# Performance work log

Measured on AMD Instinct MI355X. Metric: run time of the kernel, lower is better.

The kernel has to match this reference:

```python
import jax, jax.numpy as jnp
import numpy as np
from jax import lax

V, H, B, S, NSLOT, T, G, NSW = 20000, 400, 16, 256, 30, 10, 3, 40


def setup_inputs() -> dict:
    key = jax.random.key(0)
    ks = jax.random.split(key, 24)
    p = lambda k, shape: jax.random.normal(k, shape, dtype=jnp.float32) * 0.1
    return {
        'story': jax.random.randint(ks[0], (B, S), 0, V),
        'enc_lens': jax.random.randint(ks[1], (B,), S // 2, S + 1),
        'target_batches': jax.random.randint(ks[2], (B, NSLOT, T), 0, V),
        'domain_idx': jax.random.randint(ks[3], (NSLOT,), 0, NSW),
        'slot_idx': jax.random.randint(ks[4], (NSLOT,), 0, NSW),
        'emb': p(ks[5], (V, H)),
        'enc_Wih_f': p(ks[6], (3 * H, H)), 'enc_Whh_f': p(ks[7], (3 * H, H)),
        'enc_bih_f': p(ks[8], (3 * H,)), 'enc_bhh_f': p(ks[9], (3 * H,)),
        'enc_Wih_b': p(ks[10], (3 * H, H)), 'enc_Whh_b': p(ks[11], (3 * H, H)),
        'enc_bih_b': p(ks[12], (3 * H,)), 'enc_bhh_b': p(ks[13], (3 * H,)),
        'dec_Wih': p(ks[14], (3 * H, H)), 'dec_Whh': p(ks[15], (3 * H, H)),
        'dec_bih': p(ks[16], (3 * H,)), 'dec_bhh': p(ks[17], (3 * H,)),
        'Wr': p(ks[18], (1, 3 * H)), 'br': p(ks[19], (1,)),
        'Wg': p(ks[20], (G, H)), 'bg': p(ks[21], (G,)),
        'slot_table': p(ks[22], (NSW, H)),
    }


def _gru_scan(x, m, h0, Wih, Whh, bih, bhh):
    # x: [S,B,H], m: [S,B] validity mask (packed-sequence semantics)
    def step(h, xm):
        xt, mt = xm
        gi = xt @ Wih.T + bih
        gh = h @ Whh.T + bhh
        ir, iz, inn = jnp.split(gi, 3, -1)
        hr, hz, hn = jnp.split(gh, 3, -1)
        r = jax.nn.sigmoid(ir + hr)
        z = jax.nn.sigmoid(iz + hz)
        n = jnp.tanh(inn + r * hn)
        hnew = (1.0 - z) * n + z * h
        h = jnp.where(mt[:, None], hnew, h)
        y = jnp.where(mt[:, None], hnew, 0.0)
        return h, y
    hT, ys = lax.scan(step, h0, (x, m))
    return ys, hT


def reference(story, enc_lens, target_batches, domain_idx, slot_idx, emb,
              enc_Wih_f, enc_Whh_f, enc_bih_f, enc_bhh_f,
              enc_Wih_b, enc_Whh_b, enc_bih_b, enc_bhh_b,
              dec_Wih, dec_Whh, dec_bih, dec_bhh,
              Wr, br, Wg, bg, slot_table):
    Bc, Sc = story.shape
    nslot = domain_idx.shape[0]
    Tc = target_batches.shape[2]
    NB = nslot * Bc

    # ----- EncoderRNN: bidirectional GRU over story (seq-major) -----
    x = emb[story.T]                                   # [S,B,H]
    mask = jnp.arange(Sc)[:, None] < enc_lens[None, :]  # [S,B]
    h0 = jnp.zeros((Bc, H), jnp.float32)
    ys_f, h_f = _gru_scan(x, mask, h0, enc_Wih_f, enc_Whh_f, enc_bih_f, enc_bhh_f)
    ys_b, h_b = _gru_scan(x[::-1], mask[::-1], h0, enc_Wih_b, enc_Whh_b, enc_bih_b, enc_bhh_b)
    ys_b = ys_b[::-1]
    encoded_outputs = (ys_f + ys_b).transpose(1, 0, 2)  # [B,S,H]
    enc_hidden = h_f + h_b                              # [B,H]

    # ----- Generator (parallel decode, teacher forcing) -----
    combined = slot_table[domain_idx] + slot_table[slot_idx]           # [nslot,H]
    slot_emb_arr = jnp.repeat(combined[:, None, :], Bc, axis=1).reshape(NB, H)
    hidden0 = jnp.tile(enc_hidden, (nslot, 1))                         # [NB,H]
    enc_out = jnp.tile(encoded_outputs, (nslot, 1, 1))                 # [NB,S,H]
    lens_rep = jnp.tile(enc_lens, nslot)
    story_rep = jnp.tile(story, (nslot, 1))                            # [NB,S]
    attn_mask = jnp.arange(Sc)[None, :] < lens_rep[:, None]            # [NB,S]
    rows = jnp.arange(NB)[:, None]

    # teacher-forced decoder inputs: step0 = slot emb, then gold tokens
    tgt_flat = target_batches.transpose(1, 0, 2).reshape(NB, Tc)       # [NB,T]
    dec_in = jnp.concatenate([slot_emb_arr[None], emb[tgt_flat[:, :Tc - 1].T]], axis=0)  # [T,NB,H]

    def dec_step(h, x_in):
        gi = x_in @ dec_Wih.T + dec_bih
        gh = h @ dec_Whh.T + dec_bhh
        ir, iz, inn = jnp.split(gi, 3, -1)
        hr, hz, hn = jnp.split(gh, 3, -1)
        r = jax.nn.sigmoid(ir + hr)
        z = jax.nn.sigmoid(iz + hz)
        n = jnp.tanh(inn + r * hn)
        h = (1.0 - z) * n + z * h                      # dec_state == new hidden
        scores = jnp.einsum('nh,nsh->ns', h, enc_out)
        scores = jnp.where(attn_mask, scores, -jnp.inf)
        prob = jax.nn.softmax(scores, axis=1)          # [NB,S]
        context = jnp.einsum('ns,nsh->nh', prob, enc_out)
        p_vocab = jax.nn.softmax(h @ emb.T, axis=1)    # [NB,V]
        p_gen_vec = jnp.concatenate([h, context, x_in], axis=-1)
        sw = jax.nn.sigmoid(p_gen_vec @ Wr.T + br)     # [NB,1]
        p_ctx = jnp.zeros_like(p_vocab).at[rows, story_rep].add(prob)
        final_p = (1.0 - sw) * p_ctx + sw * p_vocab
        return h, (final_p, context)

    _, (finals, contexts) = lax.scan(dec_step, hidden0, dec_in)
    all_point_outputs = finals.reshape(Tc, nslot, Bc, V).transpose(1, 2, 0, 3)  # [nslot,B,T,V]
    all_gate_outputs = (contexts[0] @ Wg.T + bg).reshape(nslot, Bc, G)
    return all_point_outputs, all_gate_outputs
```

## Files before the change

### kernel.cpp

```cpp
#include <hip/hip_runtime.h>
#include <hip/hip_bf16.h>

typedef unsigned short u16;
typedef __attribute__((ext_vector_type(8))) short bf16x8;
typedef __attribute__((ext_vector_type(4))) float f32x4;
typedef __attribute__((ext_vector_type(4))) unsigned u32x4;

static constexpr int V = 20000, H = 400, B = 16, S = 256, NSLOT = 30, T = 10, G = 3;
static constexpr int H3 = 3 * H;
static constexpr int NB = NSLOT * B;
static constexpr int MM = T * NB;
static constexpr int ENBLK = 20;
static constexpr int ESL   = 20;
static constexpr int EROWS = 64;
static constexpr int EKP   = 416;
static constexpr int ENC_BLOCKS = 2 * ENBLK;
static constexpr int DGI_TM = (MM + 63) / 64;
static constexpr int DGI_TN = (H3 + 63) / 64;
static constexpr int DGI_TILES = DGI_TM * DGI_TN;
static constexpr int DGH_TM = (NB + 63) / 64;
static constexpr int DGH_TN = (H3 + 63) / 64;
static constexpr int DGH_TILES = DGH_TM * DGH_TN;
static constexpr int HP2 = 424;
static constexpr int SCP = 260;
static constexpr int PP  = 264;
static constexpr int CXP = 404;
static constexpr int FUSED_LDS = 32*HP2*2 + 32*SCP*4 + 32*PP*2 + 32*CXP*4;
static constexpr int NE = V * H;
static constexpr int NW = H3 * H;
static constexpr int NP = 2 * ENBLK * EROWS * EKP;

__device__ __forceinline__ float bf2f(u16 v) {
    union { unsigned u; float f; } x; x.u = ((unsigned)v) << 16; return x.f;
}
__device__ __forceinline__ u16 f2bf(float f) {
    union { float f; unsigned u; } x; x.f = f;
    unsigned r = x.u + 0x7fffu + ((x.u >> 16) & 1u);
    return (u16)(r >> 16);
}
__device__ __forceinline__ float sigm(float v) { return 1.f / (1.f + __expf(-v)); }

__global__ __launch_bounds__(256) void gemm_bt(
    const u16* __restrict__ A, const u16* __restrict__ Bt,
    const float* __restrict__ bias, float* __restrict__ C,
    int M, int N, int K, int lda, int ldb, long long ldc)
{
    __shared__ u16 As[64][40];
    __shared__ u16 Bs[64][40];
    const int m0 = blockIdx.x * 64, n0 = blockIdx.y * 64;
    const int tid = threadIdx.x, wave = tid >> 6, lane = tid & 63;
    const int wm = (wave >> 1) * 32, wn = (wave & 1) * 32;
    const int srow = tid >> 2, scol = (tid & 3) * 8;
    const int fr = lane & 15, kq = lane >> 4;
    f32x4 acc[2][2];
#pragma unroll
    for (int i = 0; i < 2; ++i)
#pragma unroll
        for (int j = 0; j < 2; ++j) acc[i][j] = (f32x4){0.f, 0.f, 0.f, 0.f};

    for (int k0 = 0; k0 < K; k0 += 32) {
        {
            int gr = m0 + srow, gc = k0 + scol;
            bf16x8 v = (bf16x8){0,0,0,0,0,0,0,0};
            if (gr < M && gc + 8 <= K) v = *(const bf16x8*)(A + (long long)gr * lda + gc);
            *(bf16x8*)&As[srow][scol] = v;
        }
        {
            int gr = n0 + srow, gc = k0 + scol;
            bf16x8 v = (bf16x8){0,0,0,0,0,0,0,0};
            if (gr < N && gc + 8 <= K) v = *(const bf16x8*)(Bt + (long long)gr * ldb + gc);
            *(bf16x8*)&Bs[srow][scol] = v;
        }
        __syncthreads();
        bf16x8 af[2], bfr[2];
#pragma unroll
// ... 35 lines not shown
    const int M = S * B, N = H3, K = H;

    __shared__ u16 As[64][40];
    __shared__ u16 Bs[64][40];
    const int m0 = blockIdx.x * 64, n0 = blockIdx.y * 64;
    const int tid = threadIdx.x, wave = tid >> 6, lane = tid & 63;
    const int wm = (wave >> 1) * 32, wn = (wave & 1) * 32;
    const int srow = tid >> 2, scol = (tid & 3) * 8;
    const int fr = lane & 15, kq = lane >> 4;
    f32x4 acc[2][2];
#pragma unroll
    for (int i = 0; i < 2; ++i)
#pragma unroll
        for (int j = 0; j < 2; ++j) acc[i][j] = (f32x4){0.f, 0.f, 0.f, 0.f};

    for (int k0 = 0; k0 < K; k0 += 32) {
        {
            int gr = m0 + srow, gc = k0 + scol;
            bf16x8 v = (bf16x8){0,0,0,0,0,0,0,0};
            if (gr < M && gc + 8 <= K) v = *(const bf16x8*)(A + (long long)gr * K + gc);
            *(bf16x8*)&As[srow][scol] = v;
        }
        {
            int gr = n0 + srow, gc = k0 + scol;
            bf16x8 v = (bf16x8){0,0,0,0,0,0,0,0};
            if (gr < N && gc + 8 <= K) v = *(const bf16x8*)(Bt + (long long)gr * K + gc);
            *(bf16x8*)&Bs[srow][scol] = v;
        }
        __syncthreads();
        bf16x8 af[2], bfr[2];
#pragma unroll
        for (int i = 0; i < 2; ++i) af[i]  = *(const bf16x8*)&As[wm + i * 16 + fr][kq * 8];
#pragma unroll
        for (int j = 0; j < 2; ++j) bfr[j] = *(const bf16x8*)&Bs[wn + j * 16 + fr][kq * 8];
#pragma unroll
        for (int i = 0; i < 2; ++i)
#pragma unroll
            for (int j = 0; j < 2; ++j)
                acc[i][j] = __builtin_amdgcn_mfma_f32_16x16x32_bf16(af[i], bfr[j], acc[i][j], 0, 0, 0);
        __syncthreads();
    }

#pragma unroll
    for (int i = 0; i < 2; ++i)
#pragma unroll
        for (int j = 0; j < 2; ++j) {
            int col = n0 + wn + j * 16 + fr;
            float bv = (col < N) ? bias[col] : 0.f;
#pragma unroll
            for (int r = 0; r < 4; ++r) {
                int row = m0 + wm + i * 16 + kq * 4 + r;
                if (row < M && col < N) C[(long long)row * H3 + col] = acc[i][j][r] + bv;
            }
        }
}

__global__ __launch_bounds__(256) void vocab_rowsum_kernel(
    const u16* __restrict__ A, const u16* __restrict__ Bt,
    float* __restrict__ rowsum)
{
    __shared__ u16 As[128][40];
    __shared__ u16 Bs[128][40];
    const int m0 = blockIdx.x * 128, n0 = blockIdx.y * 128;
    const int tid = threadIdx.x, wave = tid >> 6, lane = tid & 63;
    const int wm = (wave >> 1) * 64, wn = (wave & 1) * 64;
    const int srow = tid >> 1, scol = (tid & 1) * 16;
    const int fr = lane & 15, kq = lane >> 4;
    f32x4 acc[4][4];
#pragma unroll
    for (int i = 0; i < 4; ++i)
#pragma unroll
        for (int j = 0; j < 4; ++j) acc[i][j] = (f32x4){0.f, 0.f, 0.f, 0.f};

    for (int k0 = 0; k0 < H; k0 += 32) {
        {
            int gr = m0 + srow, gc = k0 + scol;
            bf16x8 v0 = (bf16x8){0,0,0,0,0,0,0,0}, v1 = v0;
            if (gr < MM) {
                const u16* src = A + (long long)gr * H + gc;
                if (gc + 8 <= H)  v0 = *(const bf16x8*)src;
                if (gc + 16 <= H) v1 = *(const bf16x8*)(src + 8);
            }
            *(bf16x8*)&As[srow][scol] = v0;
            *(bf16x8*)&As[srow][scol + 8] = v1;
        }
        {
            int gr = n0 + srow, gc = k0 + scol;
            bf16x8 v0 = (bf16x8){0,0,0,0,0,0,0,0}, v1 = v0;
            if (gr < V) {
                const u16* src = Bt + (long long)gr * H + gc;
                if (gc + 8 <= H)  v0 = *(const bf16x8*)src;
                if (gc + 16 <= H) v1 = *(const bf16x8*)(src + 8);
            }
            *(bf16x8*)&Bs[srow][scol] = v0;
            *(bf16x8*)&Bs[srow][scol + 8] = v1;
        }
        __syncthreads();
        bf16x8 af[4], bfr[4];
#pragma unroll
        for (int i = 0; i < 4; ++i) af[i]  = *(const bf16x8*)&As[wm + i * 16 + fr][kq * 8];
#pragma unroll
        for (int j = 0; j < 4; ++j) bfr[j] = *(const bf16x8*)&Bs[wn + j * 16 + fr][kq * 8];
#pragma unroll
        for (int i = 0; i < 4; ++i)
#pragma unroll
            for (int j = 0; j < 4; ++j)
                acc[i][j] = __builtin_amdgcn_mfma_f32_16x16x32_bf16(af[i], bfr[j], acc[i][j], 0, 0, 0);
        __syncthreads();
    }

#pragma unroll
    for (int i = 0; i < 4; ++i)
#pragma unroll
        for (int r = 0; r < 4; ++r) {
            int row = m0 + wm + i * 16 + kq * 4 + r;
            float s = 0.f;
#pragma unroll
            for (int j = 0; j < 4; ++j) {
                int col = n0 + wn + j * 16 + fr;
                if (row < MM && col < V) s += __expf(acc[i][j][r]);
            }
            s += __shfl_xor(s, 1); s += __shfl_xor(s, 2);
            s += __shfl_xor(s, 4); s += __shfl_xor(s, 8);
            if (fr == 0 && row < MM) atomicAdd(&rowsum[row], s);
        }
}

__global__ __launch_bounds__(256) void vocab_write_kernel(
    const u16* __restrict__ A, const u16* __restrict__ Bt,
    const float* __restrict__ swvT, const float* __restrict__ rowsum,
    float* __restrict__ C)
{
    __shared__ u16 As[128][40];
    __shared__ u16 Bs[128][40];
    const int m0 = blockIdx.x * 128, n0 = blockIdx.y * 128;
    const int tid = threadIdx.x, wave = tid >> 6, lane = tid & 63;
    const int wm = (wave >> 1) * 64, wn = (wave & 1) * 64;
    const int srow = tid >> 1, scol = (tid & 1) * 16;
    const int fr = lane & 15, kq = lane >> 4;
    f32x4 acc[4][4];
#pragma unroll
    for (int i = 0; i < 4; ++i)
#pragma unroll
        for (int j = 0; j < 4; ++j) acc[i][j] = (f32x4){0.f, 0.f, 0.f, 0.f};

    for (int k0 = 0; k0 < H; k0 += 32) {
        {
            int gr = m0 + srow, gc = k0 + scol;
            bf16x8 v0 = (bf16x8){0,0,0,0,0,0,0,0}, v1 = v0;
            if (gr < MM) {
                const u16* src = A + (long long)gr * H + gc;
                if (gc + 8 <= H)  v0 = *(const bf16x8*)src;
                if (gc + 16 <= H) v1 = *(const bf16x8*)(src + 8);
            }
            *(bf16x8*)&As[srow][scol] = v0;
            *(bf16x8*)&As[srow][scol + 8] = v1;
        }
        {
            int gr = n0 + srow, gc = k0 + scol;
            bf16x8 v0 = (bf16x8){0,0,0,0,0,0,0,0}, v1 = v0;
            if (gr < V) {
                const u16* src = Bt + (long long)gr * H + gc;
                if (gc + 8 <= H)  v0 = *(const bf16x8*)src;
                if (gc + 16 <= H) v1 = *(const bf16x8*)(src + 8);
            }
            *(bf16x8*)&Bs[srow][scol] = v0;
            *(bf16x8*)&Bs[srow][scol + 8] = v1;
        }
        __syncthreads();
        bf16x8 af[4], bfr[4];
#pragma unroll
        for (int i = 0; i < 4; ++i) af[i]  = *(const bf16x8*)&As[wm + i * 16 + fr][kq * 8];
#pragma unroll
        for (int j = 0; j < 4; ++j) bfr[j] = *(const bf16x8*)&Bs[wn + j * 16 + fr][kq * 8];
#pragma unroll
        for (int i = 0; i < 4; ++i)
#pragma unroll
            for (int j = 0; j < 4; ++j)
                acc[i][j] = __builtin_amdgcn_mfma_f32_16x16x32_bf16(af[i], bfr[j], acc[i][j], 0, 0, 0);
        __syncthreads();
    }

#pragma unroll
    for (int i = 0; i < 4; ++i)
#pragma unroll
        for (int r = 0; r < 4; ++r) {
            int row = m0 + wm + i * 16 + kq * 4 + r;
            float f = 0.f;
            if (row < MM) f = swvT[row] / rowsum[row];
#pragma unroll
            for (int j = 0; j < 4; ++j) {
                int col = n0 + wn + j * 16 + fr;
                if (row < MM && col < V) {
                    int n = row % NB, t = row / NB;
                    C[((long long)n * T + t) * V + col] = __expf(acc[i][j][r]) * f;
                }
            }
        }
}

__global__ void prep_all_kernel(
    const float* __restrict__ emb, u16* __restrict__ embb,
    const float* __restrict__ wihf, u16* __restrict__ wihfb,
    const float* __restrict__ wihb, u16* __restrict__ wihbb,
    const float* __restrict__ dwih, u16* __restrict__ dwihb,
    const float* __restrict__ dwhh, u16* __restrict__ dwhhb,
    const float* __restrict__ whhf, const float* __restrict__ whhb,
    u16* __restrict__ wencp)
{
    const int total = NE + 4 * NW + NP;
    for (int i = blockIdx.x * blockDim.x + threadIdx.x; i < total;
         i += gridDim.x * blockDim.x) {
        if (i < NE) { embb[i] = f2bf(emb[i]); continue; }
        int i2 = i - NE;
        if (i2 < NW) { wihfb[i2] = f2bf(wihf[i2]); continue; }
        i2 -= NW;
        if (i2 < NW) { wihbb[i2] = f2bf(wihb[i2]); continue; }
        i2 -= NW;
        if (i2 < NW) { dwihb[i2] = f2bf(dwih[i2]); continue; }
        i2 -= NW;
        if (i2 < NW) { dwhhb[i2] = f2bf(dwhh[i2]); continue; }
        i2 -= NW;
        int k = i2 % EKP; int r = i2 / EKP;
        int rloc = r % EROWS; r /= EROWS;
        int j = r % ENBLK; int dir = r / ENBLK;
        u16 v = 0;
        if (k < H && rloc < 3 * ESL) {
            int g = rloc / ESL, c = rloc % ESL;
            const float* W = dir ? whhb : whhf;
            v = f2bf(W[(long long)(g * H + j * ESL + c) * H + k]);
        }
        wencp[i2] = v;
    }
}

__global__ void embed_decin_kernel(
    const int* __restrict__ story, const u16* __restrict__ embb,
    u16* __restrict__ xb,
    const int* __restrict__ tgt, const int* __restrict__ dom,
    const int* __restrict__ sidx, const float* __restrict__ slt,
    u16* __restrict__ decin)
{
    int row = blockIdx.x;
    if (row < S * B) {
        int s = row >> 4, b = row & 15;
        int tok = story[b * S + s];
        const u16* e = embb + (long long)tok * H;
        u16* d = xb + (long long)row * H;
        for (int k = threadIdx.x; k < H; k += blockDim.x) d[k] = e[k];
    } else {
        int i = row - S * B;
// ... 191 lines not shown
            float ng = tanhf(gn1 + rg * (ghn + bhn1));
            float hn = (1.f - zg) * ng + zg * h1r;
            bool msk = s < len1;
            float y = msk ? hn : 0.f;
            if (msk) h1r = hn;
            ys[((long long)(b1 * S + s)) * H + k0 + kl1] = y;
            u16 hi = f2bf(h1r);
            unsigned packed = (unsigned)hi | ((unsigned)f2bf(h1r - bf2f(hi)) << 16);
            __hip_atomic_store(&hpub[b1 * EKP + k0 + kl1], packed, __ATOMIC_RELAXED,
                               __HIP_MEMORY_SCOPE_AGENT);
        }
        __syncthreads();
        if (tid == 0)
            __hip_atomic_store(&flg_d[t * ENBLK + j], 1, __ATOMIC_RELAXED,
                               __HIP_MEMORY_SCOPE_AGENT);
    }
    ho[b0 * H + k0 + kl0] = h0r;
    if (has1) ho[b1 * H + k0 + kl1] = h1r;
}

__global__ __launch_bounds__(256) void packE_h0_kernel(
    const float* __restrict__ ysf, const float* __restrict__ ysb,
    u16* __restrict__ E, u16* __restrict__ ET,
    const float* __restrict__ hf, const float* __restrict__ hb,
    float* __restrict__ hf32, u16* __restrict__ hnk)
{
    __shared__ u16 tile[32][400];
    const int blk = blockIdx.x;
    if (blk < B * (S / 32)) {
        const int b = blk / (S / 32), s0 = (blk % (S / 32)) * 32;
        for (int si = 0; si < 32; ++si) {
            const long long base = ((long long)b * S + s0 + si) * H;
            for (int k = threadIdx.x; k < H; k += blockDim.x) {
                u16 v = f2bf(ysf[base + k] + ysb[base + k]);
                E[base + k] = v;
                tile[si][k] = v;
            }
        }
        __syncthreads();
        for (int idx = threadIdx.x; idx < 32 * H; idx += blockDim.x) {
            int k = idx >> 5, si = idx & 31;
            ET[((long long)b * H + k) * S + s0 + si] = tile[si][k];
        }
    } else {
        int n = blk - B * (S / 32), b = n & 15;
        for (int k = threadIdx.x; k < H; k += blockDim.x) {
            float v = hf[b * H + k] + hb[b * H + k];
            hf32[(long long)n * H + k] = v;
            hnk[(long long)n * H + k] = f2bf(v);
        }
    }
}

__global__ __launch_bounds__(256) void gru_cell_kernel(
    const float* __restrict__ dgi, const float* __restrict__ dgh,
    float* __restrict__ hf32, u16* __restrict__ hall, int t)
{
    const int total = NB * H;
    for (int i = blockIdx.x * 256 + threadIdx.x; i < total; i += gridDim.x * 256) {
        int n = i / H, k = i % H;
        const float* gi = dgi + ((long long)t * NB + n) * H3;
        const float* gh = dgh + (long long)n * H3;
        float r  = sigm(gi[k] + gh[k]);
        float z  = sigm(gi[H + k] + gh[H + k]);
        float nn = tanhf(gi[2 * H + k] + r * gh[2 * H + k]);
        float h  = hf32[i];
        float hn = (1.f - z) * nn + z * h;
        hf32[i] = hn;
        hall[((long long)t * NB + n) * H + k] = f2bf(hn);
    }
}

__global__ __launch_bounds__(512) void dec_attn_kernel(
    const u16* __restrict__ hall, const u16* __restrict__ dwhhb,
    const float* __restrict__ dbhh, float* __restrict__ dgh,
    const u16* __restrict__ decinb,
    const u16* __restrict__ Eb, const u16* __restrict__ ETb,
    const int* __restrict__ lens,
    const float* __restrict__ Wr, const float* __restrict__ br,
    const float* __restrict__ Wg, const float* __restrict__ bg,
    float* __restrict__ probfT, float* __restrict__ swvT,
    float* __restrict__ gout, int t)
{
    extern __shared__ char smem[];
    const int tid = threadIdx.x, wave = tid >> 6, lane = tid & 63;
    const int fr = lane & 15, kq = lane >> 4;
    const u16* hcur = hall + (long long)t * NB * H;

    if (blockIdx.x < DGH_TILES) {
        if (t == T - 1) return;
        u16* As = (u16*)smem;
        u16* Bs = As + 64 * 40;
        const int tile = blockIdx.x;
        const int m0 = (tile % DGH_TM) * 64, n0 = (tile / DGH_TM) * 64;
        const bool act = (wave < 4);
        const int wm = (wave >> 1) * 32, wn = (wave & 1) * 32;
        const int srow = tid >> 2, scol = (tid & 3) * 8;
        f32x4 acc[2][2];
#pragma unroll
        for (int i = 0; i < 2; ++i)
#pragma unroll
            for (int j = 0; j < 2; ++j) acc[i][j] = (f32x4){0.f, 0.f, 0.f, 0.f};

        for (int k0 = 0; k0 < H; k0 += 32) {
            if (tid < 256) {
                {
                    int gr = m0 + srow, gc = k0 + scol;
                    bf16x8 v = (bf16x8){0,0,0,0,0,0,0,0};
                    if (gr < NB && gc + 8 <= H) v = *(const bf16x8*)(hcur + (long long)gr * H + gc);
                    *(bf16x8*)&As[srow * 40 + scol] = v;
                }
                {
                    int gr = n0 + srow, gc = k0 + scol;
                    bf16x8 v = (bf16x8){0,0,0,0,0,0,0,0};
                    if (gr < H3 && gc + 8 <= H) v = *(const bf16x8*)(dwhhb + (long long)gr * H + gc);
                    *(bf16x8*)&Bs[srow * 40 + scol] = v;
                }
            }
            __syncthreads();
            if (act) {
                bf16x8 af[2], bfr[2];
#pragma unroll
                for (int i = 0; i < 2; ++i) af[i]  = *(const bf16x8*)&As[(wm + i * 16 + fr) * 40 + kq * 8];
#pragma unroll
                for (int j = 0; j < 2; ++j) bfr[j] = *(const bf16x8*)&Bs[(wn + j * 16 + fr) * 40 + kq * 8];
#pragma unroll
                for (int i = 0; i < 2; ++i)
#pragma unroll
                    for (int j = 0; j < 2; ++j)
                        acc[i][j] = __builtin_amdgcn_mfma_f32_16x16x32_bf16(af[i], bfr[j], acc[i][j], 0, 0, 0);
            }
            __syncthreads();
        }
        if (act) {
#pragma unroll
            for (int i = 0; i < 2; ++i)
#pragma unroll
                for (int j = 0; j < 2; ++j) {
                    int col = n0 + wn + j * 16 + fr;
                    float bv = (col < H3) ? dbhh[col] : 0.f;
#pragma unroll
                    for (int r = 0; r < 4; ++r) {
                        int row = m0 + wm + i * 16 + kq * 4 + r;
                        if (row < NB && col < H3)
                            dgh[(long long)row * H3 + col] = acc[i][j][r] + bv;
                    }
                }
        }
        return;
    }

    u16*   hls = (u16*)smem;
    float* scs = (float*)(smem + 32 * HP2 * 2);
    u16*   pls = (u16*)(smem + 32 * HP2 * 2 + 32 * SCP * 4);
    float* cxs = (float*)(smem + 32 * HP2 * 2 + 32 * SCP * 4 + 32 * PP * 2);

    const int b = blockIdx.x - DGH_TILES;
    const int len = lens[b];

    for (int i = tid; i < 32 * (HP2 - H); i += 512) {
        int r = i / (HP2 - H), c = H + i % (HP2 - H);
        hls[r * HP2 + c] = 0;
    }
    for (int i = tid; i < 2 * HP2; i += 512) hls[30 * HP2 + i] = 0;
    for (int i = tid; i < 2 * PP; i += 512) pls[30 * PP + i] = 0;

    for (int i = tid; i < 30 * H; i += 512) {
        int slot = i / H, k = i % H;
        hls[slot * HP2 + k] = hcur[((long long)(slot * 16 + b)) * H + k];
    }
    __syncthreads();

    {
        const int nt0 = wave * 2;
        f32x4 acc[2][2];
#pragma unroll
        for (int i = 0; i < 2; ++i)
#pragma unroll
            for (int jj = 0; jj < 2; ++jj) acc[i][jj] = (f32x4){0.f, 0.f, 0.f, 0.f};
        const u16* br0 = Eb + ((long long)b * S + nt0 * 16 + fr) * H + kq * 8;
        const u16* br1 = Eb + ((long long)b * S + (nt0 + 1) * 16 + fr) * H + kq * 8;
        const u16* ar0 = hls + fr * HP2 + kq * 8;
        const u16* ar1 = hls + (16 + fr) * HP2 + kq * 8;
#pragma unroll
        for (int kk = 0; kk < 13; ++kk) {
            bf16x8 av0 = *(const bf16x8*)(ar0 + kk * 32);
            bf16x8 av1 = *(const bf16x8*)(ar1 + kk * 32);
            bf16x8 bv0, bv1;
            if (kk == 12 && kq >= 2) {
                bv0 = (bf16x8){0,0,0,0,0,0,0,0}; bv1 = bv0;
            } else {
                bv0 = *(const bf16x8*)(br0 + kk * 32);
                bv1 = *(const bf16x8*)(br1 + kk * 32);
            }
            acc[0][0] = __builtin_amdgcn_mfma_f32_16x16x32_bf16(av0, bv0, acc[0][0], 0, 0, 0);
            acc[1][0] = __builtin_amdgcn_mfma_f32_16x16x32_bf16(av1, bv0, acc[1][0], 0, 0, 0);
            acc[0][1] = __builtin_amdgcn_mfma_f32_16x16x32_bf16(av0, bv1, acc[0][1], 0, 0, 0);
            acc[1][1] = __builtin_amdgcn_mfma_f32_16x16x32_bf16(av1, bv1, acc[1][1], 0, 0, 0);
        }
#pragma unroll
// ... 113 lines not shown
    const float* emb   = (const float*)d_in[5];
    const float* wihf  = (const float*)d_in[6];
    const float* whhf  = (const float*)d_in[7];
    const float* bihf  = (const float*)d_in[8];
    const float* bhhf  = (const float*)d_in[9];
    const float* wihb  = (const float*)d_in[10];
    const float* whhb  = (const float*)d_in[11];
    const float* bihb  = (const float*)d_in[12];
    const float* bhhb  = (const float*)d_in[13];
    const float* dwih  = (const float*)d_in[14];
    const float* dwhh  = (const float*)d_in[15];
    const float* dbih  = (const float*)d_in[16];
    const float* dbhh  = (const float*)d_in[17];
    const float* Wr    = (const float*)d_in[18];
    const float* br    = (const float*)d_in[19];
    const float* Wg    = (const float*)d_in[20];
    const float* bg    = (const float*)d_in[21];
    const float* slt   = (const float*)d_in[22];
    float* out = (float*)d_out;

    char* wsb = (char*)d_ws;
    size_t off = 0;
    auto alloc = [&](size_t bytes) -> char* {
        char* p = wsb + off;
        off += (bytes + 255) & ~(size_t)255;
        return p;
    };
    u16*   embb   = (u16*)alloc((size_t)V * H * 2);
    u16*   wihfb  = (u16*)alloc((size_t)H3 * H * 2);
    u16*   wihbb  = (u16*)alloc((size_t)H3 * H * 2);
    u16*   dwihb  = (u16*)alloc((size_t)H3 * H * 2);
    u16*   dwhhb  = (u16*)alloc((size_t)H3 * H * 2);
    u16*   wencp  = (u16*)alloc((size_t)2 * ENBLK * EROWS * EKP * 2);
    unsigned* hbuf = (unsigned*)alloc((size_t)2 * S * B * EKP * 4);
    int*   flags  = (int*)alloc((size_t)2 * S * ENBLK * 4);
    u16*   xb     = (u16*)alloc((size_t)S * B * H * 2);
    u16*   decinb = (u16*)alloc((size_t)T * NB * H * 2);
    float* gif    = (float*)alloc((size_t)S * B * H3 * 4);
    float* gib    = (float*)alloc((size_t)S * B * H3 * 4);
    float* dgi    = (float*)alloc((size_t)T * NB * H3 * 4);
    float* ysf    = (float*)alloc((size_t)B * S * H * 4);
    float* ysb    = (float*)alloc((size_t)B * S * H * 4);
    float* hfv    = (float*)alloc((size_t)B * H * 4);
    float* hbv    = (float*)alloc((size_t)B * H * 4);
    u16*   Eb     = (u16*)alloc((size_t)B * S * H * 2);
    u16*   ETb    = (u16*)alloc((size_t)B * H * S * 2);
    float* hf32   = (float*)alloc((size_t)NB * H * 4);
    u16*   hnk    = (u16*)alloc((size_t)NB * H * 2);
    u16*   hall   = (u16*)alloc((size_t)T * NB * H * 2);
    float* dgh    = (float*)alloc((size_t)NB * H3 * 4);
    float* probfT = (float*)alloc((size_t)T * NB * S * 4);
    float* swvT   = (float*)alloc((size_t)T * NB * 4);
    float* rowsumT = (float*)alloc((size_t)T * NB * 4);
    (void)ws_size; (void)in_sizes; (void)n_in; (void)out_size;

    hipFuncSetAttribute((const void*)dec_attn_kernel,
                        hipFuncAttributeMaxDynamicSharedMemorySize, FUSED_LDS);

    hipMemsetAsync(flags, 0, (size_t)2 * S * ENBLK * 4, stream);
    hipMemsetAsync(hbuf, 0, (size_t)2 * S * B * EKP * 4, stream);
    hipMemsetAsync(rowsumT, 0, (size_t)T * NB * 4, stream);
    prep_all_kernel<<<2048, 256, 0, stream>>>(emb, embb, wihf, wihfb, wihb, wihbb,
                                              dwih, dwihb, dwhh, dwhhb,
                                              whhf, whhb, wencp);
    embed_decin_kernel<<<S * B + T * NB, 256, 0, stream>>>(
        story, embb, xb, tgt, dom, sidx, slt, decinb);
    {
        dim3 g((S * B + 63) / 64, (H3 + 63) / 64, 2);
        gemm_xw2_kernel<<<g, 256, 0, stream>>>(xb, wihfb, wihbb, bihf, bihb, gif, gib);
    }

    enc_dgi_kernel<<<ENC_BLOCKS + DGI_TILES, 256, 0, stream>>>(
        wencp, bhhf, bhhb, gif, gib, lens, hbuf, flags, ysf, ysb, hfv, hbv,
        decinb, dwihb, dbih, dgi);
    packE_h0_kernel<<<B * (S / 32) + NB, 256, 0, stream>>>(
        ysf, ysb, Eb, ETb, hfv, hbv, hf32, hnk);

    {
        dim3 g((NB + 63) / 64, (H3 + 63) / 64);
        gemm_bt<<<g, 256, 0, stream>>>(hnk, dwhhb, dbhh, dgh, NB, H3, H, H, H, H3);
    }
    for (int t = 0; t < T; ++t) {
        gru_cell_kernel<<<750, 256, 0, stream>>>(dgi, dgh, hf32, hall, t);
        dec_attn_kernel<<<DGH_TILES + 16, 512, FUSED_LDS, stream>>>(
            hall, dwhhb, dbhh, dgh, decinb, Eb, ETb, lens,
            Wr, br, Wg, bg, probfT, swvT, out + (size_t)NB * T * V, t);
    }

    {
        dim3 g((MM + 127) / 128, (V + 127) / 128);
        vocab_rowsum_kernel<<<g, 256, 0, stream>>>(hall, embb, rowsumT);
        vocab_write_kernel<<<g, 256, 0, stream>>>(hall, embb, swvT, rowsumT, out);
    }
    { dim3 g(NB, T); scatter_all_kernel<<<g, 256, 0, stream>>>(out, story, lens, swvT, probfT); }
}
```

Before: 2.075 ms.

## Overlap vocab softmax rowsum GEMM with decoder steps instead of separate pass

Removes the standalone vocab rowsum kernel and spreads its work across the decoder loop. Each step's GRU cell kernel also computes the rowsum tiles for the previous timestep. At the last step, the idle dgh-GEMM blocks of the attention kernel compute the final timestep's rowsum. This hides the large exp-sum GEMM behind the latency-bound per-step kernels, at the cost of bigger per-step grids and possible contention with the critical-path work.

```diff
diff --git a/kernel.cpp b/kernel.cpp
--- a/kernel.cpp
+++ b/kernel.cpp
@@ -21,6 +21,10 @@
 static constexpr int DGH_TM = (NB + 63) / 64;
 static constexpr int DGH_TN = (H3 + 63) / 64;
 static constexpr int DGH_TILES = DGH_TM * DGH_TN;
+static constexpr int RS_TM = (NB + 127) / 128;
+static constexpr int RS_TN = (V + 127) / 128;
+static constexpr int RS_TILES = RS_TM * RS_TN;
+static constexpr int CELL_BLOCKS = 750;
 static constexpr int HP2 = 424;
 static constexpr int SCP = 260;
 static constexpr int PP  = 264;
@@ -162,77 +166,6 @@
                 int row = m0 + wm + i * 16 + kq * 4 + r;
                 if (row < M && col < N) C[(long long)row * H3 + col] = acc[i][j][r] + bv;
             }
-        }
-}
-
-__global__ __launch_bounds__(256) void vocab_rowsum_kernel(
-    const u16* __restrict__ A, const u16* __restrict__ Bt,
-    float* __restrict__ rowsum)
-{
-    __shared__ u16 As[128][40];
-    __shared__ u16 Bs[128][40];
-    const int m0 = blockIdx.x * 128, n0 = blockIdx.y * 128;
-    const int tid = threadIdx.x, wave = tid >> 6, lane = tid & 63;
-    const int wm = (wave >> 1) * 64, wn = (wave & 1) * 64;
-    const int srow = tid >> 1, scol = (tid & 1) * 16;
-    const int fr = lane & 15, kq = lane >> 4;
-    f32x4 acc[4][4];
-#pragma unroll
-    for (int i = 0; i < 4; ++i)
-#pragma unroll
-        for (int j = 0; j < 4; ++j) acc[i][j] = (f32x4){0.f, 0.f, 0.f, 0.f};
-
-    for (int k0 = 0; k0 < H; k0 += 32) {
-        {
-            int gr = m0 + srow, gc = k0 + scol;
-            bf16x8 v0 = (bf16x8){0,0,0,0,0,0,0,0}, v1 = v0;
-            if (gr < MM) {
-                const u16* src = A + (long long)gr * H + gc;
-                if (gc + 8 <= H)  v0 = *(const bf16x8*)src;
-                if (gc + 16 <= H) v1 = *(const bf16x8*)(src + 8);
-            }
-            *(bf16x8*)&As[srow][scol] = v0;
-            *(bf16x8*)&As[srow][scol + 8] = v1;
-        }
-        {
-            int gr = n0 + srow, gc = k0 + scol;
-            bf16x8 v0 = (bf16x8){0,0,0,0,0,0,0,0}, v1 = v0;
-            if (gr < V) {
-                const u16* src = Bt + (long long)gr * H + gc;
-                if (gc + 8 <= H)  v0 = *(const bf16x8*)src;
-                if (gc + 16 <= H) v1 = *(const bf16x8*)(src + 8);
-            }
-            *(bf16x8*)&Bs[srow][scol] = v0;
-            *(bf16x8*)&Bs[srow][scol + 8] = v1;
-        }
-        __syncthreads();
-        bf16x8 af[4], bfr[4];
-#pragma unroll
-        for (int i = 0; i < 4; ++i) af[i]  = *(const bf16x8*)&As[wm + i * 16 + fr][kq * 8];
-#pragma unroll
-        for (int j = 0; j < 4; ++j) bfr[j] = *(const bf16x8*)&Bs[wn + j * 16 + fr][kq * 8];
-#pragma unroll
-        for (int i = 0; i < 4; ++i)
-#pragma unroll
-            for (int j = 0; j < 4; ++j)
-                acc[i][j] = __builtin_amdgcn_mfma_f32_16x16x32_bf16(af[i], bfr[j], acc[i][j], 0, 0, 0);
-        __syncthreads();
-    }
-
-#pragma unroll
-    for (int i = 0; i < 4; ++i)
-#pragma unroll
-        for (int r = 0; r < 4; ++r) {
-            int row = m0 + wm + i * 16 + kq * 4 + r;
-            float s = 0.f;
-#pragma unroll
-            for (int j = 0; j < 4; ++j) {
-                int col = n0 + wn + j * 16 + fr;
-                if (row < MM && col < V) s += __expf(acc[i][j][r]);
-            }
-            s += __shfl_xor(s, 1); s += __shfl_xor(s, 2);
-            s += __shfl_xor(s, 4); s += __shfl_xor(s, 8);
-            if (fr == 0 && row < MM) atomicAdd(&rowsum[row], s);
         }
 }
 
@@ -604,35 +537,108 @@
     }
 }
 
-__global__ __launch_bounds__(256) void gru_cell_kernel(
+__global__ __launch_bounds__(256) void cell_rowsum_kernel(
     const float* __restrict__ dgi, const float* __restrict__ dgh,
-    float* __restrict__ hf32, u16* __restrict__ hall, int t)
+    float* __restrict__ hf32, u16* __restrict__ hall,
+    const u16* __restrict__ embb, float* __restrict__ rowsumT, int t)
 {
-    const int total = NB * H;
-    for (int i = blockIdx.x * 256 + threadIdx.x; i < total; i += gridDim.x * 256) {
-        int n = i / H, k = i % H;
-        const float* gi = dgi + ((long long)t * NB + n) * H3;
-        const float* gh = dgh + (long long)n * H3;
-        float r  = sigm(gi[k] + gh[k]);
-        float z  = sigm(gi[H + k] + gh[H + k]);
-        float nn = tanhf(gi[2 * H + k] + r * gh[2 * H + k]);
-        float h  = hf32[i];
-        float hn = (1.f - z) * nn + z * h;
-        hf32[i] = hn;
-        hall[((long long)t * NB + n) * H + k] = f2bf(hn);
-    }
+    if (blockIdx.x < CELL_BLOCKS) {
+        const int total = NB * H;
+        for (int i = blockIdx.x * 256 + threadIdx.x; i < total; i += CELL_BLOCKS * 256) {
+            int n = i / H, k = i % H;
+            const float* gi = dgi + ((long long)t * NB + n) * H3;
+            const float* gh = dgh + (long long)n * H3;
+            float r  = sigm(gi[k] + gh[k]);
+            float z  = sigm(gi[H + k] + gh[H + k]);
+            float nn = tanhf(gi[2 * H + k] + r * gh[2 * H + k]);
+            float h  = hf32[i];
+            float hn = (1.f - z) * nn + z * h;
+            hf32[i] = hn;
+            hall[((long long)t * NB + n) * H + k] = f2bf(hn);
+        }
+        return;
+    }
+    if (t == 0) return;
+    __shared__ u16 As[128][40];
+    __shared__ u16 Bs[128][40];
+    const int tile = blockIdx.x - CELL_BLOCKS;
+    const int m0l = (tile % RS_TM) * 128, n0 = (tile / RS_TM) * 128;
+    const u16* A = hall + (long long)(t - 1) * NB * H;
+    float* rowsum = rowsumT + (long long)(t - 1) * NB;
+    const int tid = threadIdx.x, wave = tid >> 6, lane = tid & 63;
+    const int wm = (wave >> 1) * 64, wn = (wave & 1) * 64;
+    const int srow = tid >> 1, scol = (tid & 1) * 16;
+    const int fr = lane & 15, kq = lane >> 4;
+    f32x4 acc[4][4];
+#pragma unroll
+    for (int i = 0; i < 4; ++i)
+#pragma unroll
+        for (int j = 0; j < 4; ++j) acc[i][j] = (f32x4){0.f, 0.f, 0.f, 0.f};
+
+    for (int k0 = 0; k0 < H; k0 += 32) {
+        {
+            int gr = m0l + srow, gc = k0 + scol;
+            bf16x8 v0 = (bf16x8){0,0,0,0,0,0,0,0}, v1 = v0;
+            if (gr < NB) {
+                const u16* src = A + (long long)gr * H + gc;
+                if (gc + 8 <= H)  v0 = *(const bf16x8*)src;
+                if (gc + 16 <= H) v1 = *(const bf16x8*)(src + 8);
+            }
+            *(bf16x8*)&As[srow][scol] = v0;
+            *(bf16x8*)&As[srow][scol + 8] = v1;
+        }
+        {
+            int gr = n0 + srow, gc = k0 + scol;
+            bf16x8 v0 = (bf16x8){0,0,0,0,0,0,0,0}, v1 = v0;
+            if (gr < V) {
+                const u16* src = embb + (long long)gr * H + gc;
+                if (gc + 8 <= H)  v0 = *(const bf16x8*)src;
+                if (gc + 16 <= H) v1 = *(const bf16x8*)(src + 8);
+            }
+            *(bf16x8*)&Bs[srow][scol] = v0;
+            *(bf16x8*)&Bs[srow][scol + 8] = v1;
+        }
+        __syncthreads();
+        bf16x8 af[4], bfr[4];
+#pragma unroll
+        for (int i = 0; i < 4; ++i) af[i]  = *(const bf16x8*)&As[wm + i * 16 + fr][kq * 8];
+#pragma unroll
+        for (int j = 0; j < 4; ++j) bfr[j] = *(const bf16x8*)&Bs[wn + j * 16 + fr][kq * 8];
+#pragma unroll
+        for (int i = 0; i < 4; ++i)
+#pragma unroll
+            for (int j = 0; j < 4; ++j)
+                acc[i][j] = __builtin_amdgcn_mfma_f32_16x16x32_bf16(af[i], bfr[j], acc[i][j], 0, 0, 0);
+        __syncthreads();
+    }
+
+#pragma unroll
+    for (int i = 0; i < 4; ++i)
+#pragma unroll
+        for (int r = 0; r < 4; ++r) {
+            int row = m0l + wm + i * 16 + kq * 4 + r;
+            float s = 0.f;
+#pragma unroll
+            for (int j = 0; j < 4; ++j) {
+                int col = n0 + wn + j * 16 + fr;
+                if (row < NB && col < V) s += __expf(acc[i][j][r]);
+            }
+            s += __shfl_xor(s, 1); s += __shfl_xor(s, 2);
+            s += __shfl_xor(s, 4); s += __shfl_xor(s, 8);
+            if (fr == 0 && row < NB) atomicAdd(&rowsum[row], s);
+        }
 }
 
 __global__ __launch_bounds__(512) void dec_attn_kernel(
     const u16* __restrict__ hall, const u16* __restrict__ dwhhb,
     const float* __restrict__ dbhh, float* __restrict__ dgh,
-    const u16* __restrict__ decinb,
+    const u16* __restrict__ decinb, const u16* __restrict__ embb,
     const u16* __restrict__ Eb, const u16* __restrict__ ETb,
     const int* __restrict__ lens,
     const float* __restrict__ Wr, const float* __restrict__ br,
     const float* __restrict__ Wg, const float* __restrict__ bg,
     float* __restrict__ probfT, float* __restrict__ swvT,
-    float* __restrict__ gout, int t)
+    float* __restrict__ rowsumT, float* __restrict__ gout, int t)
 {
     extern __shared__ char smem[];
     const int tid = threadIdx.x, wave = tid >> 6, lane = tid & 63;
@@ -640,64 +646,139 @@
     const u16* hcur = hall + (long long)t * NB * H;
 
     if (blockIdx.x < DGH_TILES) {
-        if (t == T - 1) return;
-        u16* As = (u16*)smem;
-        u16* Bs = As + 64 * 40;
-        const int tile = blockIdx.x;
-        const int m0 = (tile % DGH_TM) * 64, n0 = (tile / DGH_TM) * 64;
-        const bool act = (wave < 4);
-        const int wm = (wave >> 1) * 32, wn = (wave & 1) * 32;
-        const int srow = tid >> 2, scol = (tid & 3) * 8;
-        f32x4 acc[2][2];
-#pragma unroll
-        for (int i = 0; i < 2; ++i)
-#pragma unroll
-            for (int j = 0; j < 2; ++j) acc[i][j] = (f32x4){0.f, 0.f, 0.f, 0.f};
-
-        for (int k0 = 0; k0 < H; k0 += 32) {
-            if (tid < 256) {
-                {
-                    int gr = m0 + srow, gc = k0 + scol;
-                    bf16x8 v = (bf16x8){0,0,0,0,0,0,0,0};
-                    if (gr < NB && gc + 8 <= H) v = *(const bf16x8*)(hcur + (long long)gr * H + gc);
-                    *(bf16x8*)&As[srow * 40 + scol] = v;
-                }
-                {
-                    int gr = n0 + srow, gc = k0 + scol;
-                    bf16x8 v = (bf16x8){0,0,0,0,0,0,0,0};
-                    if (gr < H3 && gc + 8 <= H) v = *(const bf16x8*)(dwhhb + (long long)gr * H + gc);
-                    *(bf16x8*)&Bs[srow * 40 + scol] = v;
-                }
-            }
-            __syncthreads();
-            if (act) {
-                bf16x8 af[2], bfr[2];
-#pragma unroll
-                for (int i = 0; i < 2; ++i) af[i]  = *(const bf16x8*)&As[(wm + i * 16 + fr) * 40 + kq * 8];
-#pragma unroll
-                for (int j = 0; j < 2; ++j) bfr[j] = *(const bf16x8*)&Bs[(wn + j * 16 + fr) * 40 + kq * 8];
-#pragma unroll
-                for (int i = 0; i < 2; ++i)
-#pragma unroll
-                    for (int j = 0; j < 2; ++j)
-                        acc[i][j] = __builtin_amdgcn_mfma_f32_16x16x32_bf16(af[i], bfr[j], acc[i][j], 0, 0, 0);
-            }
-            __syncthreads();
-        }
-        if (act) {
+        if (t < T - 1) {
+            u16* As = (u16*)smem;
+            u16* Bs = As + 64 * 40;
+            const int tile = blockIdx.x;
+            const int m0 = (tile % DGH_TM) * 64, n0 = (tile / DGH_TM) * 64;
+            const bool act = (wave < 4);
+            const int wm = (wave >> 1) * 32, wn = (wave & 1) * 32;
+            const int srow = tid >> 2, scol = (tid & 3) * 8;
+            f32x4 acc[2][2];
 #pragma unroll
             for (int i = 0; i < 2; ++i)
 #pragma unroll
-                for (int j = 0; j < 2; ++j) {
-                    int col = n0 + wn + j * 16 + fr;
-                    float bv = (col < H3) ? dbhh[col] : 0.f;
-#pragma unroll
-                    for (int r = 0; r < 4; ++r) {
-                        int row = m0 + wm + i * 16 + kq * 4 + r;
-                        if (row < NB && col < H3)
-                            dgh[(long long)row * H3 + col] = acc[i][j][r] + bv;
+                for (int j = 0; j < 2; ++j) acc[i][j] = (f32x4){0.f, 0.f, 0.f, 0.f};
+
+            for (int k0 = 0; k0 < H; k0 += 32) {
+                if (tid < 256) {
+                    {
+                        int gr = m0 + srow, gc = k0 + scol;
+                        bf16x8 v = (bf16x8){0,0,0,0,0,0,0,0};
+                        if (gr < NB && gc + 8 <= H) v = *(const bf16x8*)(hcur + (long long)gr * H + gc);
+                        *(bf16x8*)&As[srow * 40 + scol] = v;
+                    }
+                    {
+                        int gr = n0 + srow, gc = k0 + scol;
+                        bf16x8 v = (bf16x8){0,0,0,0,0,0,0,0};
+                        if (gr < H3 && gc + 8 <= H) v = *(const bf16x8*)(dwhhb + (long long)gr * H + gc);
+                        *(bf16x8*)&Bs[srow * 40 + scol] = v;
                     }
                 }
+                __syncthreads();
+                if (act) {
+                    bf16x8 af[2], bfr[2];
+#pragma unroll
+                    for (int i = 0; i < 2; ++i) af[i]  = *(const bf16x8*)&As[(wm + i * 16 + fr) * 40 + kq * 8];
+#pragma unroll
+                    for (int j = 0; j < 2; ++j) bfr[j] = *(const bf16x8*)&Bs[(wn + j * 16 + fr) * 40 + kq * 8];
+#pragma unroll
+                    for (int i = 0; i < 2; ++i)
+#pragma unroll
+                        for (int j = 0; j < 2; ++j)
+                            acc[i][j] = __builtin_amdgcn_mfma_f32_16x16x32_bf16(af[i], bfr[j], acc[i][j], 0, 0, 0);
+                }
+                __syncthreads();
+            }
+            if (act) {
+#pragma unroll
+                for (int i = 0; i < 2; ++i)
+#pragma unroll
+                    for (int j = 0; j < 2; ++j) {
+                        int col = n0 + wn + j * 16 + fr;
+                        float bv = (col < H3) ? dbhh[col] : 0.f;
+#pragma unroll
+                        for (int r = 0; r < 4; ++r) {
+                            int row = m0 + wm + i * 16 + kq * 4 + r;
+                            if (row < NB && col < H3)
+                                dgh[(long long)row * H3 + col] = acc[i][j][r] + bv;
+                        }
+                    }
+            }
+            return;
+        }
+        u16* As = (u16*)smem;
+        u16* Bs = As + 128 * 40;
+        const u16* A = hcur;
+        float* rowsum = rowsumT + (long long)t * NB;
+        const bool act = (wave < 4);
+        const int wm = (wave >> 1) * 64, wn = (wave & 1) * 64;
+        const int srow = tid >> 1, scol = (tid & 1) * 16;
+        for (int tile = blockIdx.x; tile < RS_TILES; tile += DGH_TILES) {
+            const int m0l = (tile % RS_TM) * 128, n0 = (tile / RS_TM) * 128;
+            f32x4 acc[4][4];
+#pragma unroll
+            for (int i = 0; i < 4; ++i)
+#pragma unroll
+                for (int j = 0; j < 4; ++j) acc[i][j] = (f32x4){0.f, 0.f, 0.f, 0.f};
+            for (int k0 = 0; k0 < H; k0 += 32) {
+                if (tid < 256) {
+                    {
+                        int gr = m0l + srow, gc = k0 + scol;
+                        bf16x8 v0 = (bf16x8){0,0,0,0,0,0,0,0}, v1 = v0;
+                        if (gr < NB) {
+                            const u16* src = A + (long long)gr * H + gc;
+                            if (gc + 8 <= H)  v0 = *(const bf16x8*)src;
+                            if (gc + 16 <= H) v1 = *(const bf16x8*)(src + 8);
+                        }
+                        *(bf16x8*)&As[srow * 40 + scol] = v0;
+                        *(bf16x8*)&As[srow * 40 + scol + 8] = v1;
+                    }
+                    {
+                        int gr = n0 + srow, gc = k0 + scol;
+                        bf16x8 v0 = (bf16x8){0,0,0,0,0,0,0,0}, v1 = v0;
+                        if (gr < V) {
+                            const u16* src = embb + (long long)gr * H + gc;
+                            if (gc + 8 <= H)  v0 = *(const bf16x8*)src;
+                            if (gc + 16 <= H) v1 = *(const bf16x8*)(src + 8);
+                        }
+                        *(bf16x8*)&Bs[srow * 40 + scol] = v0;
+                        *(bf16x8*)&Bs[srow * 40 + scol + 8] = v1;
+                    }
+                }
+                __syncthreads();
+                if (act) {
+                    bf16x8 af[4], bfr[4];
+#pragma unroll
+                    for (int i = 0; i < 4; ++i) af[i]  = *(const bf16x8*)&As[(wm + i * 16 + fr) * 40 + kq * 8];
+#pragma unroll
+                    for (int j = 0; j < 4; ++j) bfr[j] = *(const bf16x8*)&Bs[(wn + j * 16 + fr) * 40 + kq * 8];
+#pragma unroll
+                    for (int i = 0; i < 4; ++i)
+#pragma unroll
+                        for (int j = 0; j < 4; ++j)
+                            acc[i][j] = __builtin_amdgcn_mfma_f32_16x16x32_bf16(af[i], bfr[j], acc[i][j], 0, 0, 0);
+                }
+                __syncthreads();
+            }
+            if (act) {
+#pragma unroll
+                for (int i = 0; i < 4; ++i)
+#pragma unroll
+                    for (int r = 0; r < 4; ++r) {
+                        int row = m0l + wm + i * 16 + kq * 4 + r;
+                        float s = 0.f;
+#pragma unroll
+                        for (int j = 0; j < 4; ++j) {
+                            int col = n0 + wn + j * 16 + fr;
+                            if (row < NB && col < V) s += __expf(acc[i][j][r]);
+                        }
+                        s += __shfl_xor(s, 1); s += __shfl_xor(s, 2);
+                        s += __shfl_xor(s, 4); s += __shfl_xor(s, 8);
+                        if (fr == 0 && row < NB) atomicAdd(&rowsum[row], s);
+                    }
+            }
+            __syncthreads();
         }
         return;
     }
@@ -946,15 +1027,16 @@
         gemm_bt<<<g, 256, 0, stream>>>(hnk, dwhhb, dbhh, dgh, NB, H3, H, H, H, H3);
     }
     for (int t = 0; t < T; ++t) {
-        gru_cell_kernel<<<750, 256, 0, stream>>>(dgi, dgh, hf32, hall, t);
+        cell_rowsum_kernel<<<CELL_BLOCKS + RS_TILES, 256, 0, stream>>>(
+            dgi, dgh, hf32, hall, embb, rowsumT, t);
         dec_attn_kernel<<<DGH_TILES + 16, 512, FUSED_LDS, stream>>>(
-            hall, dwhhb, dbhh, dgh, decinb, Eb, ETb, lens,
-            Wr, br, Wg, bg, probfT, swvT, out + (size_t)NB * T * V, t);
+            hall, dwhhb, dbhh, dgh, decinb, embb, Eb, ETb, lens,
+            Wr, br, Wg, bg, probfT, swvT, rowsumT,
+            out + (size_t)NB * T * V, t);
     }
 
     {
         dim3 g((MM + 127) / 128, (V + 127) / 128);
-        vocab_rowsum_kernel<<<g, 256, 0, stream>>>(hall, embb, rowsumT);
         vocab_write_kernel<<<g, 256, 0, stream>>>(hall, embb, swvT, rowsumT, out);
     }
     { dim3 g(NB, T); scatter_all_kernel<<<g, 256, 0, stream>>>(out, story, lens, swvT, probfT); }
```

Result: slower. 2.419 ms (+16.6%).

## Merge vocab rowsum and write passes into one kernel with per-row-block counters

Applied to the files above, without the earlier changes.

Replaces the separate vocab rowsum and vocab write launches with a single launch. The first half of the blocks compute the exp row sums and bump a per-row-block counter. The second half spin until their row block's counter reaches the tile count, then recompute the GEMM and write normalized probabilities. This removes a launch boundary and lets write tiles for finished row blocks overlap with rowsum tiles for others. It risks deadlock if waiting blocks occupy all CUs before producers get scheduled, and uses relaxed atomics with only a compiler barrier for memory ordering.

```diff
diff --git a/kernel.cpp b/kernel.cpp
--- a/kernel.cpp
+++ b/kernel.cpp
@@ -21,6 +21,9 @@
 static constexpr int DGH_TM = (NB + 63) / 64;
 static constexpr int DGH_TN = (H3 + 63) / 64;
 static constexpr int DGH_TILES = DGH_TM * DGH_TN;
+static constexpr int RSA_TM = (MM + 127) / 128;
+static constexpr int RSA_TN = (V + 127) / 128;
+static constexpr int RSA_TILES = RSA_TM * RSA_TN;
 static constexpr int HP2 = 424;
 static constexpr int SCP = 260;
 static constexpr int PP  = 264;
@@ -165,17 +168,32 @@
         }
 }
 
-__global__ __launch_bounds__(256) void vocab_rowsum_kernel(
+__global__ __launch_bounds__(256) void vocab_ab_kernel(
     const u16* __restrict__ A, const u16* __restrict__ Bt,
-    float* __restrict__ rowsum)
+    const float* __restrict__ swvT, float* __restrict__ rowsum,
+    int* __restrict__ vcnt, float* __restrict__ C)
 {
     __shared__ u16 As[128][40];
     __shared__ u16 Bs[128][40];
-    const int m0 = blockIdx.x * 128, n0 = blockIdx.y * 128;
+    const bool isA = blockIdx.x < RSA_TILES;
+    const int tile = isA ? blockIdx.x : blockIdx.x - RSA_TILES;
+    const int mb = tile / RSA_TN, nt = tile % RSA_TN;
+    const int m0 = mb * 128, n0 = nt * 128;
     const int tid = threadIdx.x, wave = tid >> 6, lane = tid & 63;
     const int wm = (wave >> 1) * 64, wn = (wave & 1) * 64;
     const int srow = tid >> 1, scol = (tid & 1) * 16;
     const int fr = lane & 15, kq = lane >> 4;
+
+    if (!isA) {
+        if (tid == 0) {
+            while (__hip_atomic_load(&vcnt[mb], __ATOMIC_RELAXED,
+                                     __HIP_MEMORY_SCOPE_AGENT) < RSA_TN)
+                __builtin_amdgcn_s_sleep(4);
+        }
+        __syncthreads();
+        asm volatile("" ::: "memory");
+    }
+
     f32x4 acc[4][4];
 #pragma unroll
     for (int i = 0; i < 4; ++i)
@@ -219,94 +237,44 @@
         __syncthreads();
     }
 
-#pragma unroll
-    for (int i = 0; i < 4; ++i)
-#pragma unroll
-        for (int r = 0; r < 4; ++r) {
-            int row = m0 + wm + i * 16 + kq * 4 + r;
-            float s = 0.f;
-#pragma unroll
-            for (int j = 0; j < 4; ++j) {
-                int col = n0 + wn + j * 16 + fr;
-                if (row < MM && col < V) s += __expf(acc[i][j][r]);
-            }
-            s += __shfl_xor(s, 1); s += __shfl_xor(s, 2);
-            s += __shfl_xor(s, 4); s += __shfl_xor(s, 8);
-            if (fr == 0 && row < MM) atomicAdd(&rowsum[row], s);
-        }
-}
-
-__global__ __launch_bounds__(256) void vocab_write_kernel(
-    const u16* __restrict__ A, const u16* __restrict__ Bt,
-    const float* __restrict__ swvT, const float* __restrict__ rowsum,
-    float* __restrict__ C)
-{
-    __shared__ u16 As[128][40];
-    __shared__ u16 Bs[128][40];
-    const int m0 = blockIdx.x * 128, n0 = blockIdx.y * 128;
-    const int tid = threadIdx.x, wave = tid >> 6, lane = tid & 63;
-    const int wm = (wave >> 1) * 64, wn = (wave & 1) * 64;
-    const int srow = tid >> 1, scol = (tid & 1) * 16;
-    const int fr = lane & 15, kq = lane >> 4;
-    f32x4 acc[4][4];
-#pragma unroll
-    for (int i = 0; i < 4; ++i)
-#pragma unroll
-        for (int j = 0; j < 4; ++j) acc[i][j] = (f32x4){0.f, 0.f, 0.f, 0.f};
-
-    for (int k0 = 0; k0 < H; k0 += 32) {
-        {
-            int gr = m0 + srow, gc = k0 + scol;
-            bf16x8 v0 = (bf16x8){0,0,0,0,0,0,0,0}, v1 = v0;
-            if (gr < MM) {
-                const u16* src = A + (long long)gr * H + gc;
-                if (gc + 8 <= H)  v0 = *(const bf16x8*)src;
-                if (gc + 16 <= H) v1 = *(const bf16x8*)(src + 8);
-            }
-            *(bf16x8*)&As[srow][scol] = v0;
-            *(bf16x8*)&As[srow][scol + 8] = v1;
-        }
-        {
-            int gr = n0 + srow, gc = k0 + scol;
-            bf16x8 v0 = (bf16x8){0,0,0,0,0,0,0,0}, v1 = v0;
-            if (gr < V) {
-                const u16* src = Bt + (long long)gr * H + gc;
-                if (gc + 8 <= H)  v0 = *(const bf16x8*)src;
-                if (gc + 16 <= H) v1 = *(const bf16x8*)(src + 8);
-            }
-            *(bf16x8*)&Bs[srow][scol] = v0;
-            *(bf16x8*)&Bs[srow][scol + 8] = v1;
-        }
-        __syncthreads();
-        bf16x8 af[4], bfr[4];
-#pragma unroll
-        for (int i = 0; i < 4; ++i) af[i]  = *(const bf16x8*)&As[wm + i * 16 + fr][kq * 8];
-#pragma unroll
-        for (int j = 0; j < 4; ++j) bfr[j] = *(const bf16x8*)&Bs[wn + j * 16 + fr][kq * 8];
+    if (isA) {
 #pragma unroll
         for (int i = 0; i < 4; ++i)
 #pragma unroll
-            for (int j = 0; j < 4; ++j)
-                acc[i][j] = __builtin_amdgcn_mfma_f32_16x16x32_bf16(af[i], bfr[j], acc[i][j], 0, 0, 0);
-        __syncthreads();
-    }
-
-#pragma unroll
-    for (int i = 0; i < 4; ++i)
-#pragma unroll
-        for (int r = 0; r < 4; ++r) {
-            int row = m0 + wm + i * 16 + kq * 4 + r;
-            float f = 0.f;
-            if (row < MM) f = swvT[row] / rowsum[row];
-#pragma unroll
-            for (int j = 0; j < 4; ++j) {
-                int col = n0 + wn + j * 16 + fr;
-                if (row < MM && col < V) {
-                    int n = row % NB, t = row / NB;
-                    C[((long long)n * T + t) * V + col] = __expf(acc[i][j][r]) * f;
+            for (int r = 0; r < 4; ++r) {
+                int row = m0 + wm + i * 16 + kq * 4 + r;
+                float s = 0.f;
+#pragma unroll
+                for (int j = 0; j < 4; ++j) {
+                    int col = n0 + wn + j * 16 + fr;
+                    if (row < MM && col < V) s += __expf(acc[i][j][r]);
                 }
-            }
-        }
+                s += __shfl_xor(s, 1); s += __shfl_xor(s, 2);
+                s += __shfl_xor(s, 4); s += __shfl_xor(s, 8);
+                if (fr == 0 && row < MM) atomicAdd(&rowsum[row], s);
+            }
+        __syncthreads();
+        if (tid == 0)
+            __hip_atomic_fetch_add(&vcnt[mb], 1, __ATOMIC_RELAXED,
+                                   __HIP_MEMORY_SCOPE_AGENT);
+    } else {
+#pragma unroll
+        for (int i = 0; i < 4; ++i)
+#pragma unroll
+            for (int r = 0; r < 4; ++r) {
+                int row = m0 + wm + i * 16 + kq * 4 + r;
+                float f = 0.f;
+                if (row < MM) f = swvT[row] / rowsum[row];
+#pragma unroll
+                for (int j = 0; j < 4; ++j) {
+                    int col = n0 + wn + j * 16 + fr;
+                    if (row < MM && col < V) {
+                        int n = row % NB, t = row / NB;
+                        C[((long long)n * T + t) * V + col] = __expf(acc[i][j][r]) * f;
+                    }
+                }
+            }
+    }
 }
 
 __global__ void prep_all_kernel(
@@ -917,6 +885,7 @@
     float* probfT = (float*)alloc((size_t)T * NB * S * 4);
     float* swvT   = (float*)alloc((size_t)T * NB * 4);
     float* rowsumT = (float*)alloc((size_t)T * NB * 4);
+    int*   vcnt   = (int*)alloc((size_t)RSA_TM * 4);
     (void)ws_size; (void)in_sizes; (void)n_in; (void)out_size;
 
     hipFuncSetAttribute((const void*)dec_attn_kernel,
@@ -925,6 +894,7 @@
     hipMemsetAsync(flags, 0, (size_t)2 * S * ENBLK * 4, stream);
     hipMemsetAsync(hbuf, 0, (size_t)2 * S * B * EKP * 4, stream);
     hipMemsetAsync(rowsumT, 0, (size_t)T * NB * 4, stream);
+    hipMemsetAsync(vcnt, 0, (size_t)RSA_TM * 4, stream);
     prep_all_kernel<<<2048, 256, 0, stream>>>(emb, embb, wihf, wihfb, wihb, wihbb,
                                               dwih, dwihb, dwhh, dwhhb,
                                               whhf, whhb, wencp);
@@ -952,10 +922,7 @@
             Wr, br, Wg, bg, probfT, swvT, out + (size_t)NB * T * V, t);
     }
 
-    {
-        dim3 g((MM + 127) / 128, (V + 127) / 128);
-        vocab_rowsum_kernel<<<g, 256, 0, stream>>>(hall, embb, rowsumT);
-        vocab_write_kernel<<<g, 256, 0, stream>>>(hall, embb, swvT, rowsumT, out);
-    }
+    vocab_ab_kernel<<<2 * RSA_TILES, 256, 0, stream>>>(
+        hall, embb, swvT, rowsumT, vcnt, out);
     { dim3 g(NB, T); scatter_all_kernel<<<g, 256, 0, stream>>>(out, story, lens, swvT, probfT); }
 }
```

Measured after the change: 2.349 ms. 13.2% more time.
